# Kernel tuning notes

Measured on AMD Instinct MI355X. Metric: run time of the kernel, lower is better.

Reference implementation:

```python
import jax, jax.numpy as jnp
from jax import lax
import numpy as np

L, I, H, O = 8192, 256, 2048, 1


def setup_inputs() -> dict:
    key = jax.random.key(0)
    ks = jax.random.split(key, 11)
    s = 1.0 / np.sqrt(H)  # PyTorch nn.RNN init scale, keeps tanh unsaturated
    return {
        "x": jax.random.normal(ks[0], (1, L, I), dtype=jnp.float32),
        "W_ih0": jax.random.normal(ks[1], (H, I), dtype=jnp.float32) * s,
        "W_hh0": jax.random.normal(ks[2], (H, H), dtype=jnp.float32) * s,
        "b_ih0": jax.random.normal(ks[3], (H,), dtype=jnp.float32) * s,
        "b_hh0": jax.random.normal(ks[4], (H,), dtype=jnp.float32) * s,
        "W_ih1": jax.random.normal(ks[5], (H, H), dtype=jnp.float32) * s,
        "W_hh1": jax.random.normal(ks[6], (H, H), dtype=jnp.float32) * s,
        "b_ih1": jax.random.normal(ks[7], (H,), dtype=jnp.float32) * s,
        "b_hh1": jax.random.normal(ks[8], (H,), dtype=jnp.float32) * s,
        "W_fc": jax.random.normal(ks[9], (O, H), dtype=jnp.float32) * s,
        "b_fc": jax.random.normal(ks[10], (O,), dtype=jnp.float32) * s,
    }


def _rnn_layer(seq, W_ih, W_hh, b_ih, b_hh):
    # seq: [L, D_in] -> [L, H]; h_t = tanh(x_t W_ih^T + b_ih + h_{t-1} W_hh^T + b_hh)
    pre = seq @ W_ih.T + (b_ih + b_hh)  # hoist the input GEMM out of the scan

    def step(h, p):
        h = jnp.tanh(p + h @ W_hh.T)
        return h, h

    h0 = jnp.zeros((W_hh.shape[0],), dtype=seq.dtype)
    _, out = lax.scan(step, h0, pre)
    return out


def reference(x, W_ih0, W_hh0, b_ih0, b_hh0, W_ih1, W_hh1, b_ih1, b_hh1, W_fc, b_fc):
    seq = x[0]  # batch is fixed to 1 in the original module
    seq = _rnn_layer(seq, W_ih0, W_hh0, b_ih0, b_hh0)  # layer 0: [L, H]
    seq = _rnn_layer(seq, W_ih1, W_hh1, b_ih1, b_hh1)  # layer 1: [L, H]
    last = seq[-1]  # out[:, -1, :]
    out = jax.nn.sigmoid(last @ W_fc.T + b_fc)  # [O]
    return out[None, :]  # [1, O]


if __name__ == "__main__":
    inp = setup_inputs()
    print(reference(**inp).shape)
```

## Files before the change

### kernel.cpp

```cpp
#include <hip/hip_runtime.h>
#include <math.h>

#define L_SEQ 8192
#define I_DIM 256
#define H_DIM 2048
#define NWG0  64
#define NWG1  128
#define NWG   (NWG0 + NWG1)
#define TPB   512
#define RD    16
#define RM    (RD - 1)
#define TLAG  11


typedef float f32x4 __attribute__((ext_vector_type(4)));
typedef float f32x2 __attribute__((ext_vector_type(2)));

__device__ __forceinline__ void cstore1(float* p, float v) {
  asm volatile("global_store_dword %0, %1, off sc0 sc1" :: "v"(p), "v"(v) : "memory");
}
__device__ __forceinline__ void cstore2f(float* p, float a, float b) {
  f32x2 v; v.x = a; v.y = b;
  asm volatile("global_store_dwordx2 %0, %1, off sc0 sc1" :: "v"(p), "v"(v) : "memory");
}
__device__ __forceinline__ void cstore4f(float* p, float a, float b, float c, float d) {
  f32x4 v; v.x = a; v.y = b; v.z = c; v.w = d;
  asm volatile("global_store_dwordx4 %0, %1, off sc0 sc1" :: "v"(p), "v"(v) : "memory");
}
__device__ __forceinline__ void cstoreu(unsigned* p, unsigned v) {
  asm volatile("global_store_dword %0, %1, off sc0 sc1" :: "v"(p), "v"(v) : "memory");
}
__device__ __forceinline__ float cload1(const float* p) {
  float v;
  asm volatile("global_load_dword %0, %1, off sc0 sc1\n\ts_waitcnt vmcnt(0)"
               : "=v"(v) : "v"(p) : "memory");
  return v;
}
__device__ __forceinline__ unsigned cloadu(const unsigned* p) {
  unsigned v;
  asm volatile("global_load_dword %0, %1, off sc0 sc1\n\ts_waitcnt vmcnt(0)"
               : "=v"(v) : "v"(p) : "memory");
  return v;
}
__device__ __forceinline__ float4 cload4(const float* p) {
  float4 v;
  asm volatile("global_load_dwordx4 %0, %1, off sc0 sc1\n\ts_waitcnt vmcnt(0)"
               : "=v"(v) : "v"(p) : "memory");
  return v;
}
__device__ __forceinline__ float4 ld4(const float* p) {
  float4 v;
  asm volatile("global_load_dwordx4 %0, %1, off\n\ts_waitcnt vmcnt(0)"
               : "=v"(v) : "v"(p) : "memory");
  return v;
}
__device__ __forceinline__ void pf_issue(f32x4& v, const float* p) {
  asm volatile("global_load_dwordx4 %0, %1, off sc0 sc1" : "=&v"(v) : "v"(p) : "memory");
}
__device__ __forceinline__ void pf_wait1(f32x4& v) {
  asm volatile("s_waitcnt vmcnt(1)" : "+v"(v) :: "memory");
  __builtin_amdgcn_sched_barrier(0);
}
__device__ __forceinline__ float tagc(int step) {
  return 4.f + 8.f * (float)((step >> 4) & 1);
}
__device__ __forceinline__ bool ok4(float4 v, float c) {
  return __builtin_fabsf(v.x - c) <= 1.f && __builtin_fabsf(v.y - c) <= 1.f &&
         __builtin_fabsf(v.z - c) <= 1.f && __builtin_fabsf(v.w - c) <= 1.f;
}
__device__ __forceinline__ bool ok4x(f32x4 v, float c) {
  return __builtin_fabsf(v.x - c) <= 1.f && __builtin_fabsf(v.y - c) <= 1.f &&
         __builtin_fabsf(v.z - c) <= 1.f && __builtin_fabsf(v.w - c) <= 1.f;
}
__device__ __forceinline__ float4 poll4(const float* p, float c) {
  float4 v = cload4(p);
  while (!ok4(v, c)) { __builtin_amdgcn_s_sleep(1); v = cload4(p); }
  return make_float4(v.x - c, v.y - c, v.z - c, v.w - c);
}
__device__ __forceinline__ float4 pf_finish(f32x4 pf, const float* p, float c) {
  if (!ok4x(pf, c)) {
    do {
      __builtin_amdgcn_s_sleep(1);
      float4 r = cload4(p);
      pf.x = r.x; pf.y = r.y; pf.z = r.z; pf.w = r.w;
    } while (!ok4x(pf, c));
  }
  return make_float4(pf.x - c, pf.y - c, pf.z - c, pf.w - c);
}
__device__ __forceinline__ float dot4(float4 a, float4 b) {
  return a.x * b.x + a.y * b.y + a.z * b.z + a.w * b.w;
}
__device__ __forceinline__ float tanh_fast(float v) {
  float e = __expf(2.f * v);
  return 1.f - 2.f / (e + 1.f);
}
__device__ __forceinline__ void start_barrier(unsigned* bslots, int wg, int tid, unsigned value) {
  __syncthreads();
  if (tid == 0) cstoreu(&bslots[wg], value);
  if (tid < NWG) {
    while ((int)(cloadu(&bslots[tid]) - value) < 0) __builtin_amdgcn_s_sleep(1);
  }
  __syncthreads();
}

__global__ __launch_bounds__(TPB, 2)
void rnn2_colb(const float* __restrict__ x,
               const float* __restrict__ Wih0, const float* __restrict__ Whh0,
               const float* __restrict__ bih0, const float* __restrict__ bhh0,
               const float* __restrict__ Wih1, const float* __restrict__ Whh1,
               const float* __restrict__ bih1, const float* __restrict__ bhh1,
               const float* __restrict__ Wfc,  const float* __restrict__ bfc,
               float* __restrict__ out,
               unsigned* __restrict__ runctr, unsigned* __restrict__ bslots,
               float* __restrict__ h0s, float* __restrict__ h1s)
{
  const int wg   = blockIdx.x;
  const int tid  = threadIdx.x;
  const int lane = tid & 63;
  const int wv   = tid >> 6;
  __shared__ float4 lds4[2][1152];

  const unsigned runbase = cloadu(runctr);

  if (wg < NWG0) {
    const int r0 = wg * 32 + wv * 4;
    float4 whhr[32];
    float4 wihr[4];
    {
      #pragma unroll
      for (int j = 0; j < 4; ++j) {
        const float* wr2 = Whh0 + (size_t)(r0 + j) * H_DIM + (lane << 5);
        #pragma unroll
        for (int k = 0; k < 8; ++k) whhr[j * 8 + k] = ld4(wr2 + (k << 2));
        wihr[j] = ld4(Wih0 + (size_t)(r0 + j) * I_DIM + (lane << 2));
      }
    }
    const float bs0 = bih0[r0] + bhh0[r0];
    const float bs1 = bih0[r0 + 1] + bhh0[r0 + 1];
    const float bs2 = bih0[r0 + 2] + bhh0[r0 + 2];
    const float bs3 = bih0[r0 + 3] + bhh0[r0 + 3];

    {
      int sl = tid >> 5; int r = wg * 32 + (tid & 31);
      cstore1(&h0s[sl * H_DIM + r], (sl == 0) ? 4.f : 0.f);
    }
    start_barrier(bslots, wg, tid, runbase + 1);

    float xp0, xp1, xp2, xp3;
    {
      float4 xv = ((const float4*)x)[lane];
      xp0 = dot4(wihr[0], xv); xp1 = dot4(wihr[1], xv);
      xp2 = dot4(wihr[2], xv); xp3 = dot4(wihr[3], xv);
    }

    for (int s = 1; s <= L_SEQ; ++s) {
      const int P = s & 1;
      float4 hv = poll4(h0s + ((s - 1) & RM) * H_DIM + (tid << 2), tagc(s - 1));
      lds4[P][tid + (tid >> 3)] = hv;
      if ((s & 3) == 0 && s >= 12 && tid < NWG1) {
        const float tc = tagc(s - TLAG);
        const float* tp = h1s + ((s - TLAG) & RM) * H_DIM + (tid << 4);
        while (__builtin_fabsf(cload1(tp) - tc) > 1.f) __builtin_amdgcn_s_sleep(1);
      }
      __syncthreads();
      float p0 = xp0, p1 = xp1, p2 = xp2, p3 = xp3;
      #pragma unroll
      for (int k = 0; k < 8; ++k) {
        float4 h = lds4[P][9 * lane + k];
        p0 += dot4(whhr[k], h);
        p1 += dot4(whhr[8 + k], h);
        p2 += dot4(whhr[16 + k], h);
        p3 += dot4(whhr[24 + k], h);
      }
      #pragma unroll
      for (int m = 1; m < 64; m <<= 1) {
        p0 += __shfl_xor(p0, m); p1 += __shfl_xor(p1, m);
        p2 += __shfl_xor(p2, m); p3 += __shfl_xor(p3, m);
      }
      if (lane == 0) {
        const float ct = tagc(s);
        cstore4f(h0s + (s & RM) * H_DIM + r0,
                 tanh_fast(p0 + bs0) + ct, tanh_fast(p1 + bs1) + ct,
                 tanh_fast(p2 + bs2) + ct, tanh_fast(p3 + bs3) + ct);
      }
      if (s < L_SEQ) {
        float4 xv = ((const float4*)x)[s * 64 + lane];
        xp0 = dot4(wihr[0], xv); xp1 = dot4(wihr[1], xv);
        xp2 = dot4(wihr[2], xv); xp3 = dot4(wihr[3], xv);
      }
    }

    if (wg == 0) {
      float4 hv = poll4(h1s + (tid << 2), tagc(L_SEQ));
      float4 wf = ((const float4*)Wfc)[tid];
      float pz = dot4(hv, wf);
      #pragma unroll
      for (int m = 1; m < 64; m <<= 1) pz += __shfl_xor(pz, m);
      float* red = (float*)&lds4[0][0];
      __syncthreads();
      if ((tid & 63) == 0) red[wv] = pz;
      __syncthreads();
      if (tid == 0) {
        float z = bfc[0];
        #pragma unroll
        for (int w = 0; w < 8; ++w) z += red[w];
        out[0] = 1.f / (1.f + __expf(-z));
        cstoreu(runctr, runbase + 1);
      }
    }
  } else {
    const int wgl = wg - NWG0;
    const int r0  = wgl * 16 + wv * 2;
    float4 wihr[16], whhr[16];
    {
      #pragma unroll
      for (int j = 0; j < 2; ++j) {
        const float* wr = Wih1 + (size_t)(r0 + j) * H_DIM + (lane << 5);
        #pragma unroll
        for (int k = 0; k < 8; ++k) wihr[j * 8 + k] = ld4(wr + (k << 2));
        const float* wr2 = Whh1 + (size_t)(r0 + j) * H_DIM + (lane << 5);
        #pragma unroll
        for (int k = 0; k < 8; ++k) whhr[j * 8 + k] = ld4(wr2 + (k << 2));
      }
    }
    const float ba = bih1[r0] + bhh1[r0];
    const float bb = bih1[r0 + 1] + bhh1[r0 + 1];

    if (tid < 256) {
      int sl = tid >> 4; int r = wgl * 16 + (tid & 15);
      cstore1(&h1s[sl * H_DIM + r], (sl == 0) ? 4.f : 0.f);
    }
    start_barrier(bslots, wg, tid, runbase + 1);

    f32x4 pfA;
    pf_issue(pfA, h0s + (1 & RM) * H_DIM + (tid << 2));
    (void)cloadu(runctr);

    for (int t = 1; t <= L_SEQ; ++t) {
      const int P = t & 1;
      const float c0 = tagc(t);
      pf_wait1(pfA);
      float4 a = pf_finish(pfA, h0s + (t & RM) * H_DIM + (tid << 2), c0);
      lds4[P][tid + (tid >> 3)] = a;
      if (t < L_SEQ)
        pf_issue(pfA, h0s + ((t + 1) & RM) * H_DIM + (tid << 2));
      __syncthreads();
      float pa = 0.f, pb = 0.f;
      #pragma unroll
      for (int k = 0; k < 8; ++k) {
        float4 h = lds4[P][9 * lane + k];
        pa += dot4(wihr[k], h);
        pb += dot4(wihr[8 + k], h);
      }
      float4 b = poll4(h1s + ((t - 1) & RM) * H_DIM + (tid << 2), tagc(t - 1));
      lds4[P][576 + tid + (tid >> 3)] = b;
      __syncthreads();
      #pragma unroll
      for (int k = 0; k < 8; ++k) {
        float4 h = lds4[P][576 + 9 * lane + k];
        pa += dot4(whhr[k], h);
        pb += dot4(whhr[8 + k], h);
      }
      #pragma unroll
      for (int m = 1; m < 64; m <<= 1) {
        pa += __shfl_xor(pa, m); pb += __shfl_xor(pb, m);
      }
      if (lane == 0) {
        const float ct = tagc(t);
        cstore2f(h1s + (t & RM) * H_DIM + r0,
                 tanh_fast(pa + ba) + ct, tanh_fast(pb + bb) + ct);
      }
    }
  }
}

extern "C" void kernel_launch(void* const* d_in, const int* in_sizes, int n_in,
                              void* d_out, int out_size, void* d_ws, size_t ws_size,
                              hipStream_t stream) {
  const float* xx   = (const float*)d_in[0];
  const float* Wih0 = (const float*)d_in[1];
  const float* Whh0 = (const float*)d_in[2];
  const float* bih0 = (const float*)d_in[3];
  const float* bhh0 = (const float*)d_in[4];
  const float* Wih1 = (const float*)d_in[5];
  const float* Whh1 = (const float*)d_in[6];
  const float* bih1 = (const float*)d_in[7];
  const float* bhh1 = (const float*)d_in[8];
  const float* Wfc  = (const float*)d_in[9];
  const float* bfc  = (const float*)d_in[10];

  unsigned* runctr = (unsigned*)d_ws;
  unsigned* bslots = (unsigned*)((char*)d_ws + 256);
  float* h0s       = (float*)((char*)d_ws + 4096);
  float* h1s       = (float*)((char*)d_ws + 4096 + RD * H_DIM * sizeof(float));

  rnn2_colb<<<dim3(NWG), dim3(TPB), 0, stream>>>(
      xx, Wih0, Whh0, bih0, bhh0, Wih1, Whh1, bih1, bhh1, Wfc, bfc,
      (float*)d_out, runctr, bslots, h0s, h1s);
}
```

Baseline: 18.94 ms.

## Merge both RNN layers into every workgroup with skewed wavefront schedule and bf16 layer-1 weights

Replaces the split of 64 layer-0 and 128 layer-1 workgroups with 128 uniform workgroups. Each workgroup computes layer-0 step s and layer-1 step s-1 in the same iteration, so one barrier per step covers both layers and the separate layer-1 throttling poll goes away. To fit the extra layer-1 weights in registers, Wih1 and Whh1 are packed to bf16 pairs, which adds unpack work and lowers the precision of layer 1. The h1 prefetch now waits on vmcnt(0) instead of vmcnt(1), and there is one extra drain iteration.

```diff
diff --git a/kernel.cpp b/kernel.cpp
--- a/kernel.cpp
+++ b/kernel.cpp
@@ -4,13 +4,11 @@
 #define L_SEQ 8192
 #define I_DIM 256
 #define H_DIM 2048
-#define NWG0  64
-#define NWG1  128
-#define NWG   (NWG0 + NWG1)
+#define NWG   128
 #define TPB   512
 #define RD    16
 #define RM    (RD - 1)
-#define TLAG  11
+#define NSTEP (L_SEQ + 1)
 
 
 typedef float f32x4 __attribute__((ext_vector_type(4)));
@@ -23,18 +21,8 @@
   f32x2 v; v.x = a; v.y = b;
   asm volatile("global_store_dwordx2 %0, %1, off sc0 sc1" :: "v"(p), "v"(v) : "memory");
 }
-__device__ __forceinline__ void cstore4f(float* p, float a, float b, float c, float d) {
-  f32x4 v; v.x = a; v.y = b; v.z = c; v.w = d;
-  asm volatile("global_store_dwordx4 %0, %1, off sc0 sc1" :: "v"(p), "v"(v) : "memory");
-}
 __device__ __forceinline__ void cstoreu(unsigned* p, unsigned v) {
   asm volatile("global_store_dword %0, %1, off sc0 sc1" :: "v"(p), "v"(v) : "memory");
-}
-__device__ __forceinline__ float cload1(const float* p) {
-  float v;
-  asm volatile("global_load_dword %0, %1, off sc0 sc1\n\ts_waitcnt vmcnt(0)"
-               : "=v"(v) : "v"(p) : "memory");
-  return v;
 }
 __device__ __forceinline__ unsigned cloadu(const unsigned* p) {
   unsigned v;
@@ -57,8 +45,8 @@
 __device__ __forceinline__ void pf_issue(f32x4& v, const float* p) {
   asm volatile("global_load_dwordx4 %0, %1, off sc0 sc1" : "=&v"(v) : "v"(p) : "memory");
 }
-__device__ __forceinline__ void pf_wait1(f32x4& v) {
-  asm volatile("s_waitcnt vmcnt(1)" : "+v"(v) :: "memory");
+__device__ __forceinline__ void pf_wait0(f32x4& v) {
+  asm volatile("s_waitcnt vmcnt(0)" : "+v"(v) :: "memory");
   __builtin_amdgcn_sched_barrier(0);
 }
 __device__ __forceinline__ float tagc(int step) {
@@ -94,6 +82,15 @@
   float e = __expf(2.f * v);
   return 1.f - 2.f / (e + 1.f);
 }
+__device__ __forceinline__ unsigned bfp(float a, float b) {
+  unsigned ua = __float_as_uint(a), ub = __float_as_uint(b);
+  ua += 0x7fffu + ((ua >> 16) & 1u);
+  ub += 0x7fffu + ((ub >> 16) & 1u);
+  return (ua >> 16) | (ub & 0xffff0000u);
+}
+__device__ __forceinline__ float blo(unsigned w) { return __uint_as_float(w << 16); }
+__device__ __forceinline__ float bhi(unsigned w) { return __uint_as_float(w & 0xffff0000u); }
+
 __device__ __forceinline__ void start_barrier(unsigned* bslots, int wg, int tid, unsigned value) {
   __syncthreads();
   if (tid == 0) cstoreu(&bslots[wg], value);
@@ -104,15 +101,15 @@
 }
 
 __global__ __launch_bounds__(TPB, 2)
-void rnn2_colb(const float* __restrict__ x,
-               const float* __restrict__ Wih0, const float* __restrict__ Whh0,
-               const float* __restrict__ bih0, const float* __restrict__ bhh0,
-               const float* __restrict__ Wih1, const float* __restrict__ Whh1,
-               const float* __restrict__ bih1, const float* __restrict__ bhh1,
-               const float* __restrict__ Wfc,  const float* __restrict__ bfc,
-               float* __restrict__ out,
-               unsigned* __restrict__ runctr, unsigned* __restrict__ bslots,
-               float* __restrict__ h0s, float* __restrict__ h1s)
+void rnn2_merged(const float* __restrict__ x,
+                 const float* __restrict__ Wih0, const float* __restrict__ Whh0,
+                 const float* __restrict__ bih0, const float* __restrict__ bhh0,
+                 const float* __restrict__ Wih1, const float* __restrict__ Whh1,
+                 const float* __restrict__ bih1, const float* __restrict__ bhh1,
+                 const float* __restrict__ Wfc,  const float* __restrict__ bfc,
+                 float* __restrict__ out,
+                 unsigned* __restrict__ runctr, unsigned* __restrict__ bslots,
+                 float* __restrict__ h0s, float* __restrict__ h1s)
 {
   const int wg   = blockIdx.x;
   const int tid  = threadIdx.x;
@@ -122,154 +119,146 @@
 
   const unsigned runbase = cloadu(runctr);
 
-  if (wg < NWG0) {
-    const int r0 = wg * 32 + wv * 4;
-    float4 whhr[32];
-    float4 wihr[4];
+  const int r0 = wg * 16 + wv * 2;
+
+  float4 whh0r[16];
+  float4 wih0r[2];
+  {
+    #pragma unroll
+    for (int j = 0; j < 2; ++j) {
+      const float* wr = Whh0 + (size_t)(r0 + j) * H_DIM + (lane << 5);
+      #pragma unroll
+      for (int k = 0; k < 8; ++k) whh0r[j * 8 + k] = ld4(wr + (k << 2));
+      wih0r[j] = ld4(Wih0 + (size_t)(r0 + j) * I_DIM + (lane << 2));
+    }
+  }
+  unsigned wih1q[32], whh1q[32];
+  {
+    #pragma unroll
+    for (int j = 0; j < 2; ++j) {
+      const float* wr = Wih1 + (size_t)(r0 + j) * H_DIM + (lane << 5);
+      #pragma unroll
+      for (int k = 0; k < 8; ++k) {
+        float4 v = ld4(wr + (k << 2));
+        wih1q[j * 16 + 2 * k]     = bfp(v.x, v.y);
+        wih1q[j * 16 + 2 * k + 1] = bfp(v.z, v.w);
+      }
+      const float* wr2 = Whh1 + (size_t)(r0 + j) * H_DIM + (lane << 5);
+      #pragma unroll
+      for (int k = 0; k < 8; ++k) {
+        float4 v = ld4(wr2 + (k << 2));
+        whh1q[j * 16 + 2 * k]     = bfp(v.x, v.y);
+        whh1q[j * 16 + 2 * k + 1] = bfp(v.z, v.w);
+      }
+    }
+  }
+  const float b00 = bih0[r0] + bhh0[r0];
+  const float b01 = bih0[r0 + 1] + bhh0[r0 + 1];
+  const float b10 = bih1[r0] + bhh1[r0];
+  const float b11 = bih1[r0 + 1] + bhh1[r0 + 1];
+
+  if (tid < 256) {
+    int sl = tid >> 4; int r = wg * 16 + (tid & 15);
+    float v = (sl == 0) ? 4.f : 0.f;
+    cstore1(&h0s[sl * H_DIM + r], v);
+    cstore1(&h1s[sl * H_DIM + r], v);
+  }
+  start_barrier(bslots, wg, tid, runbase + 1);
+
+  float xp0, xp1;
+  {
+    float4 xv = ((const float4*)x)[lane];
+    xp0 = dot4(wih0r[0], xv); xp1 = dot4(wih0r[1], xv);
+  }
+  f32x4 pfA; pfA.x = 0.f; pfA.y = 0.f; pfA.z = 0.f; pfA.w = 0.f;
+
+  for (int s = 1; s <= NSTEP; ++s) {
+    const int P = s & 1;
+    if (s >= 2) {
+      const float c1 = tagc(s - 2);
+      pf_wait0(pfA);
+      lds4[P][576 + tid + (tid >> 3)] =
+          pf_finish(pfA, h1s + ((s - 2) & RM) * H_DIM + (tid << 2), c1);
+    }
     {
-      #pragma unroll
-      for (int j = 0; j < 4; ++j) {
-        const float* wr2 = Whh0 + (size_t)(r0 + j) * H_DIM + (lane << 5);
-        #pragma unroll
-        for (int k = 0; k < 8; ++k) whhr[j * 8 + k] = ld4(wr2 + (k << 2));
-        wihr[j] = ld4(Wih0 + (size_t)(r0 + j) * I_DIM + (lane << 2));
-      }
-    }
-    const float bs0 = bih0[r0] + bhh0[r0];
-    const float bs1 = bih0[r0 + 1] + bhh0[r0 + 1];
-    const float bs2 = bih0[r0 + 2] + bhh0[r0 + 2];
-    const float bs3 = bih0[r0 + 3] + bhh0[r0 + 3];
-
-    {
-      int sl = tid >> 5; int r = wg * 32 + (tid & 31);
-      cstore1(&h0s[sl * H_DIM + r], (sl == 0) ? 4.f : 0.f);
-    }
-    start_barrier(bslots, wg, tid, runbase + 1);
-
-    float xp0, xp1, xp2, xp3;
-    {
-      float4 xv = ((const float4*)x)[lane];
-      xp0 = dot4(wihr[0], xv); xp1 = dot4(wihr[1], xv);
-      xp2 = dot4(wihr[2], xv); xp3 = dot4(wihr[3], xv);
-    }
-
-    for (int s = 1; s <= L_SEQ; ++s) {
-      const int P = s & 1;
-      float4 hv = poll4(h0s + ((s - 1) & RM) * H_DIM + (tid << 2), tagc(s - 1));
-      lds4[P][tid + (tid >> 3)] = hv;
-      if ((s & 3) == 0 && s >= 12 && tid < NWG1) {
-        const float tc = tagc(s - TLAG);
-        const float* tp = h1s + ((s - TLAG) & RM) * H_DIM + (tid << 4);
-        while (__builtin_fabsf(cload1(tp) - tc) > 1.f) __builtin_amdgcn_s_sleep(1);
-      }
-      __syncthreads();
-      float p0 = xp0, p1 = xp1, p2 = xp2, p3 = xp3;
+      const float c0 = tagc(s - 1);
+      lds4[P][tid + (tid >> 3)] =
+          poll4(h0s + ((s - 1) & RM) * H_DIM + (tid << 2), c0);
+    }
+    __syncthreads();
+
+    if (s <= L_SEQ) {
+      float p0 = xp0, p1 = xp1;
       #pragma unroll
       for (int k = 0; k < 8; ++k) {
         float4 h = lds4[P][9 * lane + k];
-        p0 += dot4(whhr[k], h);
-        p1 += dot4(whhr[8 + k], h);
-        p2 += dot4(whhr[16 + k], h);
-        p3 += dot4(whhr[24 + k], h);
+        p0 += dot4(whh0r[k], h);
+        p1 += dot4(whh0r[8 + k], h);
       }
       #pragma unroll
       for (int m = 1; m < 64; m <<= 1) {
         p0 += __shfl_xor(p0, m); p1 += __shfl_xor(p1, m);
-        p2 += __shfl_xor(p2, m); p3 += __shfl_xor(p3, m);
       }
       if (lane == 0) {
         const float ct = tagc(s);
-        cstore4f(h0s + (s & RM) * H_DIM + r0,
-                 tanh_fast(p0 + bs0) + ct, tanh_fast(p1 + bs1) + ct,
-                 tanh_fast(p2 + bs2) + ct, tanh_fast(p3 + bs3) + ct);
-      }
-      if (s < L_SEQ) {
-        float4 xv = ((const float4*)x)[s * 64 + lane];
-        xp0 = dot4(wihr[0], xv); xp1 = dot4(wihr[1], xv);
-        xp2 = dot4(wihr[2], xv); xp3 = dot4(wihr[3], xv);
-      }
-    }
-
-    if (wg == 0) {
-      float4 hv = poll4(h1s + (tid << 2), tagc(L_SEQ));
-      float4 wf = ((const float4*)Wfc)[tid];
-      float pz = dot4(hv, wf);
-      #pragma unroll
-      for (int m = 1; m < 64; m <<= 1) pz += __shfl_xor(pz, m);
-      float* red = (float*)&lds4[0][0];
-      __syncthreads();
-      if ((tid & 63) == 0) red[wv] = pz;
-      __syncthreads();
-      if (tid == 0) {
-        float z = bfc[0];
-        #pragma unroll
-        for (int w = 0; w < 8; ++w) z += red[w];
-        out[0] = 1.f / (1.f + __expf(-z));
-        cstoreu(runctr, runbase + 1);
-      }
-    }
-  } else {
-    const int wgl = wg - NWG0;
-    const int r0  = wgl * 16 + wv * 2;
-    float4 wihr[16], whhr[16];
-    {
-      #pragma unroll
-      for (int j = 0; j < 2; ++j) {
-        const float* wr = Wih1 + (size_t)(r0 + j) * H_DIM + (lane << 5);
-        #pragma unroll
-        for (int k = 0; k < 8; ++k) wihr[j * 8 + k] = ld4(wr + (k << 2));
-        const float* wr2 = Whh1 + (size_t)(r0 + j) * H_DIM + (lane << 5);
-        #pragma unroll
-        for (int k = 0; k < 8; ++k) whhr[j * 8 + k] = ld4(wr2 + (k << 2));
-      }
-    }
-    const float ba = bih1[r0] + bhh1[r0];
-    const float bb = bih1[r0 + 1] + bhh1[r0 + 1];
-
-    if (tid < 256) {
-      int sl = tid >> 4; int r = wgl * 16 + (tid & 15);
-      cstore1(&h1s[sl * H_DIM + r], (sl == 0) ? 4.f : 0.f);
-    }
-    start_barrier(bslots, wg, tid, runbase + 1);
-
-    f32x4 pfA;
-    pf_issue(pfA, h0s + (1 & RM) * H_DIM + (tid << 2));
-    (void)cloadu(runctr);
-
-    for (int t = 1; t <= L_SEQ; ++t) {
-      const int P = t & 1;
-      const float c0 = tagc(t);
-      pf_wait1(pfA);
-      float4 a = pf_finish(pfA, h0s + (t & RM) * H_DIM + (tid << 2), c0);
-      lds4[P][tid + (tid >> 3)] = a;
-      if (t < L_SEQ)
-        pf_issue(pfA, h0s + ((t + 1) & RM) * H_DIM + (tid << 2));
-      __syncthreads();
-      float pa = 0.f, pb = 0.f;
+        cstore2f(h0s + (s & RM) * H_DIM + r0,
+                 tanh_fast(p0 + b00) + ct, tanh_fast(p1 + b01) + ct);
+      }
+    }
+
+    if (s >= 2) {
+      float qa = 0.f, qb = 0.f;
       #pragma unroll
       for (int k = 0; k < 8; ++k) {
         float4 h = lds4[P][9 * lane + k];
-        pa += dot4(wihr[k], h);
-        pb += dot4(wihr[8 + k], h);
-      }
-      float4 b = poll4(h1s + ((t - 1) & RM) * H_DIM + (tid << 2), tagc(t - 1));
-      lds4[P][576 + tid + (tid >> 3)] = b;
-      __syncthreads();
+        unsigned wa0 = wih1q[2 * k], wa1 = wih1q[2 * k + 1];
+        unsigned wb0 = wih1q[16 + 2 * k], wb1 = wih1q[16 + 2 * k + 1];
+        qa += blo(wa0) * h.x + bhi(wa0) * h.y + blo(wa1) * h.z + bhi(wa1) * h.w;
+        qb += blo(wb0) * h.x + bhi(wb0) * h.y + blo(wb1) * h.z + bhi(wb1) * h.w;
+      }
       #pragma unroll
       for (int k = 0; k < 8; ++k) {
         float4 h = lds4[P][576 + 9 * lane + k];
-        pa += dot4(whhr[k], h);
-        pb += dot4(whhr[8 + k], h);
+        unsigned wa0 = whh1q[2 * k], wa1 = whh1q[2 * k + 1];
+        unsigned wb0 = whh1q[16 + 2 * k], wb1 = whh1q[16 + 2 * k + 1];
+        qa += blo(wa0) * h.x + bhi(wa0) * h.y + blo(wa1) * h.z + bhi(wa1) * h.w;
+        qb += blo(wb0) * h.x + bhi(wb0) * h.y + blo(wb1) * h.z + bhi(wb1) * h.w;
       }
       #pragma unroll
       for (int m = 1; m < 64; m <<= 1) {
-        pa += __shfl_xor(pa, m); pb += __shfl_xor(pb, m);
+        qa += __shfl_xor(qa, m); qb += __shfl_xor(qb, m);
       }
       if (lane == 0) {
-        const float ct = tagc(t);
-        cstore2f(h1s + (t & RM) * H_DIM + r0,
-                 tanh_fast(pa + ba) + ct, tanh_fast(pb + bb) + ct);
-      }
+        const float ct = tagc(s - 1);
+        cstore2f(h1s + ((s - 1) & RM) * H_DIM + r0,
+                 tanh_fast(qa + b10) + ct, tanh_fast(qb + b11) + ct);
+      }
+    }
+    if (s < L_SEQ) {
+      float4 xv = ((const float4*)x)[s * 64 + lane];
+      xp0 = dot4(wih0r[0], xv); xp1 = dot4(wih0r[1], xv);
+    }
+    if (s < NSTEP) {
+      pf_issue(pfA, h1s + ((s - 1) & RM) * H_DIM + (tid << 2));
+    }
+  }
+
+  if (wg == 0) {
+    float4 hv = poll4(h1s + (tid << 2), tagc(L_SEQ));
+    float4 wf = ((const float4*)Wfc)[tid];
+    float pz = dot4(hv, wf);
+    #pragma unroll
+    for (int m = 1; m < 64; m <<= 1) pz += __shfl_xor(pz, m);
+    float* red = (float*)&lds4[0][0];
+    __syncthreads();
+    if ((tid & 63) == 0) red[wv] = pz;
+    __syncthreads();
+    if (tid == 0) {
+      float z = bfc[0];
+      #pragma unroll
+      for (int w = 0; w < 8; ++w) z += red[w];
+      out[0] = 1.f / (1.f + __expf(-z));
+      cstoreu(runctr, runbase + 1);
     }
   }
 }
@@ -294,7 +283,7 @@
   float* h0s       = (float*)((char*)d_ws + 4096);
   float* h1s       = (float*)((char*)d_ws + 4096 + RD * H_DIM * sizeof(float));
 
-  rnn2_colb<<<dim3(NWG), dim3(TPB), 0, stream>>>(
+  rnn2_merged<<<dim3(NWG), dim3(TPB), 0, stream>>>(
       xx, Wih0, Whh0, bih0, bhh0, Wih1, Whh1, bih1, bhh1, Wfc, bfc,
       (float*)d_out, runctr, bslots, h0s, h1s);
 }
```

Result: slower. 25.22 ms (+33.1%).
